# Kernel tuning notes

Hardware: AMD Instinct MI355X
Metric: run time of the kernel (lower is better)

Reference implementation:

```python
import jax, jax.numpy as jnp
import numpy as np

B = 65536
OBS_DIM = 85          # input_shape
FEAT = 8              # dim_entity_feature
NL = 5                # dim_landmarks
NT = 10               # dim_total
INF = 64              # in_features == out_features
HID = 64              # rnn_hidden_dim
NACT = 5              # n_actions
ALPHA = 0.01


def _leaky(x):
    return jnp.where(x > 0, x, ALPHA * x)


def setup_inputs() -> dict:
    key = jax.random.key(0)
    ks = jax.random.split(key, 26)
    s = 0.1
    d = {
        'obs': jax.random.normal(ks[0], (B, OBS_DIM), jnp.float32),
        'hidden_state': jax.random.normal(ks[1], (B, HID), jnp.float32),
        # entity input projections (input_layer_0/1/2), stored [in, out]
        'w_in0': jax.random.normal(ks[2], (FEAT, INF), jnp.float32) * s,
        'b_in0': jax.random.normal(ks[3], (INF,), jnp.float32) * s,
        'w_in1': jax.random.normal(ks[4], (FEAT, INF), jnp.float32) * s,
        'b_in1': jax.random.normal(ks[5], (INF,), jnp.float32) * s,
        'w_in2': jax.random.normal(ks[6], (FEAT, INF), jnp.float32) * s,
        'b_in2': jax.random.normal(ks[7], (INF,), jnp.float32) * s,
        # GAT params
        'W': jax.random.normal(ks[8], (INF, INF), jnp.float32) * s,
        'a': jax.random.normal(ks[9], (2 * INF, 1), jnp.float32) * s,
        # output MLP on attention rows (dim_soft = 2*dim_nearby = 10)
        'w_o1': jax.random.normal(ks[10], (2 * NL, 32), jnp.float32) * s,
        'b_o1': jax.random.normal(ks[11], (32,), jnp.float32) * s,
        'w_o2': jax.random.normal(ks[12], (32, 16), jnp.float32) * s,
        'b_o2': jax.random.normal(ks[13], (16,), jnp.float32) * s,
        'w_o3': jax.random.normal(ks[14], (16, 1), jnp.float32) * s,
        'b_o3': jax.random.normal(ks[15], (1,), jnp.float32) * s,
        # fc1 takes obs (85) concat atom_plug (5) -> 90
        'w_fc1': jax.random.normal(ks[16], (OBS_DIM + NL, HID), jnp.float32) * s,
        'b_fc1': jax.random.normal(ks[17], (HID,), jnp.float32) * s,
        # GRUCell, torch layout: [3H, in]
        'w_ih': jax.random.normal(ks[18], (3 * HID, HID), jnp.float32) * s,
        'w_hh': jax.random.normal(ks[19], (3 * HID, HID), jnp.float32) * s,
        'b_ih': jax.random.normal(ks[20], (3 * HID,), jnp.float32) * s,
        'b_hh': jax.random.normal(ks[21], (3 * HID,), jnp.float32) * s,
        'w_fc2': jax.random.normal(ks[22], (HID, NACT), jnp.float32) * s,
        'b_fc2': jax.random.normal(ks[23], (NACT,), jnp.float32) * s,
    }
    return d


def reference(obs, hidden_state, w_in0, b_in0, w_in1, b_in1, w_in2, b_in2,
              W, a, w_o1, b_o1, w_o2, b_o2, w_o3, b_o3,
              w_fc1, b_fc1, w_ih, w_hh, b_ih, b_hh, w_fc2, b_fc2):
    # data_preprocess: drop last dim_nearby cols, rotate first 4 to back, reshape to entities
    o = obs[:, :OBS_DIM - NL]                               # [B, 80]
    obs_in = jnp.concatenate([o[:, 4:], o[:, :4]], axis=-1).reshape(-1, NT, FEAT)  # [B,10,8]

    h0 = _leaky(obs_in @ w_in0 + b_in0)                     # [B,10,64]
    h1 = _leaky(obs_in @ w_in1 + b_in1)
    h2 = _leaky(obs_in @ w_in2 + b_in2)
    h_mix = jnp.concatenate([h0[:, :NL], h1[:, NL:NT - 1], h2[:, NT - 1:NT]], axis=1)  # [B,10,64]

    Wh = h_mix @ W                                          # [B,10,64]
    Wh1 = Wh @ a[:INF]                                      # [B,10,1]
    Wh2 = Wh @ a[INF:]                                      # [B,10,1]
    e = _leaky(Wh1 + jnp.swapaxes(Wh2, 1, 2))               # [B,10,10]

    att0 = jax.nn.softmax(e[:, :NL, NL:], axis=-1)          # [B,5,5]
    att1 = jnp.swapaxes(jax.nn.softmax(e[:, NL:, :NL], axis=-1), 1, 2)  # [B,5,5]
    attention = jnp.concatenate([att0, att1], axis=-1)      # [B,5,10]

    hp = _leaky(attention @ w_o1 + b_o1)
    hp = _leaky(hp @ w_o2 + b_o2)
    hp = _leaky(hp @ w_o3 + b_o3)[..., 0]                   # [B,5]
    obs_out = jax.nn.softmax(hp, axis=-1)                   # [B,5]

    obs_comb = jnp.concatenate([obs, obs_out], axis=-1)     # [B,90]
    x = jax.nn.relu(obs_comb @ w_fc1 + b_fc1)               # [B,64]

    h_in = hidden_state.reshape(-1, HID)
    gi = x @ w_ih.T + b_ih                                  # [B,192]
    gh = h_in @ w_hh.T + b_hh
    r = jax.nn.sigmoid(gi[:, :HID] + gh[:, :HID])
    z = jax.nn.sigmoid(gi[:, HID:2 * HID] + gh[:, HID:2 * HID])
    n = jnp.tanh(gi[:, 2 * HID:] + r * gh[:, 2 * HID:])
    h = (1.0 - z) * n + z * h_in                            # [B,64]

    q = h @ w_fc2 + b_fc2                                   # [B,5]
    return (q, h)
```

## Files before the change

kernel.cpp:

```cpp
#include <hip/hip_runtime.h>
#include <math.h>

namespace {

typedef __bf16 bf16x8 __attribute__((ext_vector_type(8)));
typedef __bf16 bf16x4 __attribute__((ext_vector_type(4)));
typedef float  f32x4  __attribute__((ext_vector_type(4)));
typedef float  f32x2  __attribute__((ext_vector_type(2)));

typedef __attribute__((address_space(1))) const char GChar;
typedef __attribute__((address_space(3))) char LChar;

constexpr int B_      = 65536;
constexpr int OBS_DIM_= 85;
constexpr int NL_     = 5;
constexpr int NT_     = 10;
constexpr int HID_    = 64;
constexpr int NACT_   = 5;
constexpr float ALPHA_= 0.01f;

__device__ __forceinline__ float leaky(float x)    { return fmaf(fminf(x, 0.0f), ALPHA_ - 1.0f, x); }
__device__ __forceinline__ float sigmoidf(float x) { return 1.0f / (1.0f + __expf(-x)); }
__device__ __forceinline__ float tanh_fast(float x){ return 1.0f - 2.0f / (__expf(2.0f * x) + 1.0f); }

__global__ void prep_kernel(const float* __restrict__ W, const float* __restrict__ a,
                            const float* __restrict__ w_ih, const float* __restrict__ w_hh,
                            const float* __restrict__ w_fc1, void* __restrict__ ws) {
  float* Wa   = (float*)ws;
  __bf16* ih  = (__bf16*)((char*)ws + 512);
  __bf16* hh  = ih + 192 * 64;
  __bf16* f1t = hh + 192 * 64;
  const int tid = blockIdx.x * 256 + threadIdx.x;
  if (blockIdx.x == 0 && threadIdx.x < 64) {
    const int i = threadIdx.x;
    float s1 = 0.0f, s2 = 0.0f;
    #pragma unroll
    for (int j = 0; j < 64; ++j) {
      float w = W[i * 64 + j];
      s1 += w * a[j];
      s2 += w * a[64 + j];
    }
    Wa[i] = s1;
    Wa[64 + i] = s2;
  }
  const int stride = gridDim.x * 256;
  for (int i = tid; i < 192 * 64; i += stride) {
    int pr = i >> 6, k = i & 63;
    int g  = pr >> 6;
    int q  = pr & 63;
    int orig = (g << 6) + ((q & 15) << 2) + (q >> 4);
    ih[i] = (__bf16)w_ih[orig * 64 + k];
    hh[i] = (__bf16)w_hh[orig * 64 + k];
  }
  for (int i = tid; i < 64 * 96; i += stride) {
    int n = i / 96, k = i - 96 * n;
    f1t[i] = (__bf16)(k < 90 ? w_fc1[k * 64 + n] : 0.0f);
  }
}

constexpr int SXH_ = 72;

__global__ __launch_bounds__(256, 2) void fused_kernel(
    const float* __restrict__ obs, const float* __restrict__ hidden,
    const float* __restrict__ w_in0, const float* __restrict__ b_in0,
    const float* __restrict__ w_in1, const float* __restrict__ b_in1,
    const float* __restrict__ w_in2, const float* __restrict__ b_in2,
    const float* __restrict__ w_o1, const float* __restrict__ b_o1,
    const float* __restrict__ w_o2, const float* __restrict__ b_o2,
    const float* __restrict__ w_o3, const float* __restrict__ b_o3,
    const float* __restrict__ b_fc1,
    const float* __restrict__ b_ih, const float* __restrict__ b_hh,
    const float* __restrict__ w_fc2, const float* __restrict__ b_fc2,
    const void* __restrict__ wsv,
    float* __restrict__ q_out, float* __restrict__ h_out) {

  __shared__ __align__(16) char smem[39168];
  float* s_obs = (float*)smem;
  float  (*s_att)[5][10] = (float (*)[5][10])(smem + 21760);
  __bf16 (*s_h1)[5][32]  = (__bf16 (*)[5][32])(smem + 24960);
  float  (*s_h2)[5][16]  = (float (*)[5][16])(smem + 30080);
  __bf16* A_x            = (__bf16*)(smem + 21760);
  float (*s_wh1)[12]     = (float (*)[12])(smem + 35200);
  float (*s_wh2)[12]     = (float (*)[12])(smem + 35968);
  float (*s_colm)[6]     = (float (*)[6])(smem + 36736);
  float (*s_cols)[6]     = (float (*)[6])(smem + 37120);
  float (*s_hp)[6]       = (float (*)[6])(smem + 37504);
  float* s_o5            = (float*)(smem + 37888);

  const int tid  = threadIdx.x;
  const int wv   = tid >> 6;
  const int lane = tid & 63;
  const int l16  = lane & 15;
  const int grp  = tid >> 4;
  const long gr0 = (long)blockIdx.x * 64;

  const float* Wa = (const float*)wsv;
  const __bf16* Wih = (const __bf16*)((const char*)wsv + 512);
  const __bf16* Whh = Wih + 192 * 64;
  const __bf16* Wf1 = Whh + 192 * 64;

  {
    const char* gbase = (const char*)(obs + gr0 * OBS_DIM_) + wv * 5440;
    char* lbase = smem + wv * 5440;
    #pragma unroll
    for (int j = 0; j < 5; ++j)
      __builtin_amdgcn_global_load_lds((const GChar*)(gbase + j * 1024 + lane * 16),
                                       (LChar*)(lbase + j * 1024 + lane * 16), 16, 0, 0);
    if (lane < 20)
      __builtin_amdgcn_global_load_lds((const GChar*)(gbase + 5120 + lane * 16),
                                       (LChar*)(lbase + 5120 + lane * 16), 16, 0, 0);
  }

  const int u0 = l16 * 4;
  const f32x4 wa1 = *(const f32x4*)&Wa[u0];
  const f32x4 wa2 = *(const f32x4*)&Wa[64 + u0];

  asm volatile("s_waitcnt vmcnt(0)" ::: "memory");
  __syncthreads();

  #pragma unroll 1
  for (int pass = 0; pass < 4; ++pass) {
    const int row = pass * 16 + grp;
    const float* orow = s_obs + row * OBS_DIM_;

    f32x4 wA[8];
    f32x4 bA;
    #pragma unroll
    for (int t = 0; t < NT_; ++t) {
      if (t == 0) {
        #pragma unroll
        for (int f = 0; f < 8; ++f) wA[f] = *(const f32x4*)&w_in0[f * 64 + u0];
        bA = *(const f32x4*)&b_in0[u0];
      }
      if (t == 5) {
        #pragma unroll
        for (int f = 0; f < 8; ++f) wA[f] = *(const f32x4*)&w_in1[f * 64 + u0];
        bA = *(const f32x4*)&b_in1[u0];
      }
      if (t == 9) {
        #pragma unroll
        for (int f = 0; f < 8; ++f) wA[f] = *(const f32x4*)&w_in2[f * 64 + u0];
        bA = *(const f32x4*)&b_in2[u0];
      }
      const int ia = t * 8 + 4;
      int ib = t * 8 + 8;
      if (ib >= 80) ib = 0;
      float oa[4], ob[4];
      #pragma unroll
      for (int e = 0; e < 4; ++e) { oa[e] = orow[ia + e]; ob[e] = orow[ib + e]; }
      f32x4 z = bA;
      #pragma unroll
      for (int f = 0; f < 4; ++f) {
        z[0] += oa[f] * wA[f][0]; z[1] += oa[f] * wA[f][1];
        z[2] += oa[f] * wA[f][2]; z[3] += oa[f] * wA[f][3];
      }
      #pragma unroll
      for (int f = 4; f < 8; ++f) {
        z[0] += ob[f - 4] * wA[f][0]; z[1] += ob[f - 4] * wA[f][1];
        z[2] += ob[f - 4] * wA[f][2]; z[3] += ob[f - 4] * wA[f][3];
      }
      float h0 = leaky(z[0]), h1 = leaky(z[1]), h2 = leaky(z[2]), h3 = leaky(z[3]);
      float p1t = h0 * wa1[0] + h1 * wa1[1] + h2 * wa1[2] + h3 * wa1[3];
      float p2t = h0 * wa2[0] + h1 * wa2[1] + h2 * wa2[2] + h3 * wa2[3];
      p1t += __shfl_xor(p1t, 1, 64);  p2t += __shfl_xor(p2t, 1, 64);
      p1t += __shfl_xor(p1t, 2, 64);  p2t += __shfl_xor(p2t, 2, 64);
      p1t += __shfl_xor(p1t, 4, 64);  p2t += __shfl_xor(p2t, 4, 64);
      p1t += __shfl_xor(p1t, 8, 64);  p2t += __shfl_xor(p2t, 8, 64);
      if (l16 == 0) { s_wh1[grp][t] = p1t; s_wh2[grp][t] = p2t; }
    }

    if (l16 >= 5 && l16 < 10) {
      const int jj = l16 - 5;
      float w1v = s_wh1[grp][NL_ + jj];
      float ev[NL_], m = -1e30f;
      #pragma unroll
      for (int k = 0; k < NL_; ++k) { ev[k] = leaky(w1v + s_wh2[grp][k]); m = fmaxf(m, ev[k]); }
      float s = 0.0f;
      #pragma unroll
      for (int k = 0; k < NL_; ++k) s += __expf(ev[k] - m);
      s_colm[grp][jj] = m;
      s_cols[grp][jj] = s;
    }

    if (l16 < NL_) {
      const int r = l16;
      const float wh1_r = s_wh1[grp][r];
      const float wh2_r = s_wh2[grp][r];
      float ev[NL_], m = -1e30f;
      #pragma unroll
      for (int j = 0; j < NL_; ++j) { ev[j] = leaky(wh1_r + s_wh2[grp][NL_ + j]); m = fmaxf(m, ev[j]); }
      float a0[NL_], s = 0.0f;
      #pragma unroll
      for (int j = 0; j < NL_; ++j) { a0[j] = __expf(ev[j] - m); s += a0[j]; }
      float inv = 1.0f / s;
      #pragma unroll
      for (int j = 0; j < NL_; ++j) s_att[grp][r][j] = a0[j] * inv;
      #pragma unroll
      for (int jj = 0; jj < NL_; ++jj) {
        float e = leaky(s_wh1[grp][NL_ + jj] + wh2_r);
        s_att[grp][r][NL_ + jj] = __expf(e - s_colm[grp][jj]) / s_cols[grp][jj];
      }
    }

    {
      f32x2 w1c[NT_];
      #pragma unroll
      for (int k = 0; k < NT_; ++k) w1c[k] = *(const f32x2*)&w_o1[k * 32 + l16 * 2];
      const f32x2 b1 = *(const f32x2*)&b_o1[l16 * 2];
      #pragma unroll
      for (int r5 = 0; r5 < NL_; ++r5) {
        float za = b1[0], zb = b1[1];
        #pragma unroll
        for (int k2 = 0; k2 < 5; ++k2) {
          f32x2 at = *(const f32x2*)&s_att[grp][r5][k2 * 2];
          za += at[0] * w1c[2 * k2][0] + at[1] * w1c[2 * k2 + 1][0];
          zb += at[0] * w1c[2 * k2][1] + at[1] * w1c[2 * k2 + 1][1];
        }
        s_h1[grp][r5][l16 * 2]     = (__bf16)leaky(za);
        s_h1[grp][r5][l16 * 2 + 1] = (__bf16)leaky(zb);
      }
    }

    {
      float w2c[32];
      #pragma unroll
      for (int k = 0; k < 32; ++k) w2c[k] = w_o2[k * 16 + l16];
      const float b2 = b_o2[l16];
      #pragma unroll
      for (int r5 = 0; r5 < NL_; ++r5) {
        float z = b2;
        #pragma unroll
        for (int k4 = 0; k4 < 8; ++k4) {
          bf16x4 hv = *(const bf16x4*)&s_h1[grp][r5][k4 * 4];
          z += (float)hv[0] * w2c[4 * k4] + (float)hv[1] * w2c[4 * k4 + 1]
             + (float)hv[2] * w2c[4 * k4 + 2] + (float)hv[3] * w2c[4 * k4 + 3];
        }
        s_h2[grp][r5][l16] = leaky(z);
      }
    }

    if (l16 < NL_) {
      float z3 = b_o3[0];
      #pragma unroll
      for (int k4 = 0; k4 < 4; ++k4) {
        f32x4 hv = *(const f32x4*)&s_h2[grp][l16][k4 * 4];
        z3 += hv[0] * w_o3[4 * k4] + hv[1] * w_o3[4 * k4 + 1]
            + hv[2] * w_o3[4 * k4 + 2] + hv[3] * w_o3[4 * k4 + 3];
      }
      float hp_own = leaky(z3);
      s_hp[grp][l16] = hp_own;
      float m5 = -1e30f;
      #pragma unroll
      for (int j = 0; j < NL_; ++j) m5 = fmaxf(m5, s_hp[grp][j]);
      float ssum = 0.0f;
      #pragma unroll
      for (int j = 0; j < NL_; ++j) ssum += __expf(s_hp[grp][j] - m5);
      s_o5[row * NL_ + l16] = __expf(hp_own - m5) / ssum;
    }
  }

  __syncthreads();

  const int l    = l16;
  const int quad = lane >> 4;
  const int r0   = wv * 16;

  bf16x8 ah[2];
  {
    const float* hrow_g = hidden + (gr0 + r0 + l) * HID_;
    f32x4 vha0 = *(const f32x4*)&hrow_g[quad * 8];
    f32x4 vha1 = *(const f32x4*)&hrow_g[quad * 8 + 4];
    f32x4 vhb0 = *(const f32x4*)&hrow_g[32 + quad * 8];
    f32x4 vhb1 = *(const f32x4*)&hrow_g[32 + quad * 8 + 4];
    bf16x8 t;
    t[0] = (__bf16)vha0[0]; t[1] = (__bf16)vha0[1]; t[2] = (__bf16)vha0[2]; t[3] = (__bf16)vha0[3];
    t[4] = (__bf16)vha1[0]; t[5] = (__bf16)vha1[1]; t[6] = (__bf16)vha1[2]; t[7] = (__bf16)vha1[3];
    ah[0] = t;
    t[0] = (__bf16)vhb0[0]; t[1] = (__bf16)vhb0[1]; t[2] = (__bf16)vhb0[2]; t[3] = (__bf16)vhb0[3];
    t[4] = (__bf16)vhb1[0]; t[5] = (__bf16)vhb1[1]; t[6] = (__bf16)vhb1[2]; t[7] = (__bf16)vhb1[3];
    ah[1] = t;
  }

  const f32x4 zero4 = {0.0f, 0.0f, 0.0f, 0.0f};
  const float* myrow = s_obs + (r0 + l) * OBS_DIM_;
  const float* myo5  = s_o5 + (r0 + l) * NL_;

  f32x4 cx[4];
  #pragma unroll
  for (int nt = 0; nt < 4; ++nt) cx[nt] = zero4;
  #pragma unroll
  for (int ks = 0; ks < 3; ++ks) {
    bf16x8 af;
    if (ks < 2) {
      const int cb = ks * 32 + quad * 8;
      #pragma unroll
      for (int j = 0; j < 8; ++j) af[j] = (__bf16)myrow[cb + j];
    } else {
      if (quad < 2) {
        const int cb = 64 + quad * 8;
        #pragma unroll
        for (int j = 0; j < 8; ++j) af[j] = (__bf16)myrow[cb + j];
      } else if (quad == 2) {
        #pragma unroll
        for (int j = 0; j < 5; ++j) af[j] = (__bf16)myrow[80 + j];
        #pragma unroll
        for (int j = 5; j < 8; ++j) af[j] = (__bf16)myo5[j - 5];
      } else {
        af[0] = (__bf16)myo5[3];
        af[1] = (__bf16)myo5[4];
        #pragma unroll
        for (int j = 2; j < 8; ++j) af[j] = (__bf16)0.0f;
      }
    }
    #pragma unroll
    for (int nt = 0; nt < 4; ++nt) {
      bf16x8 bf = *(const bf16x8*)&Wf1[(nt * 16 + l) * 96 + ks * 32 + quad * 8];
      cx[nt] = __builtin_amdgcn_mfma_f32_16x16x32_bf16(af, bf, cx[nt], 0, 0, 0);
    }
  }
  #pragma unroll
  for (int nt = 0; nt < 4; ++nt) {
    float bias = b_fc1[nt * 16 + l];
    #pragma unroll
    for (int rg = 0; rg < 4; ++rg) {
      float xv = fmaxf(cx[nt][rg] + bias, 0.0f);
      A_x[(r0 + quad * 4 + rg) * SXH_ + nt * 16 + l] = (__bf16)xv;
    }
  }

  bf16x8 ax[2];
  #pragma unroll
  for (int ks = 0; ks < 2; ++ks)
    ax[ks] = *(const bf16x8*)&A_x[(r0 + l) * SXH_ + ks * 32 + quad * 8];

  f32x4 cr[4], ch[4];
  #pragma unroll
  for (int nt = 0; nt < 4; ++nt) { cr[nt] = zero4; ch[nt] = zero4; }
  #pragma unroll
  for (int nt = 0; nt < 4; ++nt) {
    #pragma unroll
    for (int ks = 0; ks < 2; ++ks) {
      bf16x8 bi = *(const bf16x8*)&Wih[(nt * 16 + l) * 64 + ks * 32 + quad * 8];
      cr[nt] = __builtin_amdgcn_mfma_f32_16x16x32_bf16(ax[ks], bi, cr[nt], 0, 0, 0);
      bf16x8 bh = *(const bf16x8*)&Whh[(nt * 16 + l) * 64 + ks * 32 + quad * 8];
      cr[nt] = __builtin_amdgcn_mfma_f32_16x16x32_bf16(ah[ks], bh, cr[nt], 0, 0, 0);
    }
    #pragma unroll
    for (int ks = 0; ks < 2; ++ks) {
      bf16x8 bh = *(const bf16x8*)&Whh[(128 + nt * 16 + l) * 64 + ks * 32 + quad * 8];
      ch[nt] = __builtin_amdgcn_mfma_f32_16x16x32_bf16(ah[ks], bh, ch[nt], 0, 0, 0);
    }
  }
  f32x4 rn[4];
  {
    f32x4 a0 = *(const f32x4*)&b_ih[4 * l];
    f32x4 a1 = *(const f32x4*)&b_hh[4 * l];
    f32x4 br4 = a0 + a1;
    f32x4 bhn4 = *(const f32x4*)&b_hh[128 + 4 * l];
    #pragma unroll
    for (int nt = 0; nt < 4; ++nt)
      #pragma unroll
      for (int rg = 0; rg < 4; ++rg) {
        float rr = sigmoidf(cr[nt][rg] + br4[nt]);
        rn[nt][rg] = rr * (ch[nt][rg] + bhn4[nt]);
      }
  }

  f32x4 cn[4];
  #pragma unroll
  for (int nt = 0; nt < 4; ++nt) cn[nt] = zero4;
  #pragma unroll
  for (int nt = 0; nt < 4; ++nt)
    #pragma unroll
    for (int ks = 0; ks < 2; ++ks) {
      bf16x8 bi = *(const bf16x8*)&Wih[(128 + nt * 16 + l) * 64 + ks * 32 + quad * 8];
      cn[nt] = __builtin_amdgcn_mfma_f32_16x16x32_bf16(ax[ks], bi, cn[nt], 0, 0, 0);
    }
  f32x4 nn[4];
  {
    f32x4 bin4 = *(const f32x4*)&b_ih[128 + 4 * l];
    #pragma unroll
    for (int nt = 0; nt < 4; ++nt)
      #pragma unroll
      for (int rg = 0; rg < 4; ++rg)
        nn[nt][rg] = tanh_fast(cn[nt][rg] + bin4[nt] + rn[nt][rg]);
  }

  f32x4 cz[4];
  #pragma unroll
  for (int nt = 0; nt < 4; ++nt) cz[nt] = zero4;
  #pragma unroll
  for (int nt = 0; nt < 4; ++nt)
    #pragma unroll
    for (int ks = 0; ks < 2; ++ks) {
      bf16x8 bi = *(const bf16x8*)&Wih[(64 + nt * 16 + l) * 64 + ks * 32 + quad * 8];
      cz[nt] = __builtin_amdgcn_mfma_f32_16x16x32_bf16(ax[ks], bi, cz[nt], 0, 0, 0);
      bf16x8 bh = *(const bf16x8*)&Whh[(64 + nt * 16 + l) * 64 + ks * 32 + quad * 8];
      cz[nt] = __builtin_amdgcn_mfma_f32_16x16x32_bf16(ah[ks], bh, cz[nt], 0, 0, 0);
    }

  const long grow = gr0 + r0 + quad * 4;
  f32x4 bz4;
  {
    f32x4 a0 = *(const f32x4*)&b_ih[64 + 4 * l];
    f32x4 a1 = *(const f32x4*)&b_hh[64 + 4 * l];
    bz4 = a0 + a1;
  }
  f32x4 w20[5];
  #pragma unroll
  for (int j = 0; j < 5; ++j) w20[j] = *(const f32x4*)&w_fc2[20 * l + 4 * j];

  #pragma unroll
  for (int rg = 0; rg < 4; ++rg) {
    f32x4 hold = *(const f32x4*)&hidden[(grow + rg) * HID_ + 4 * l];
    f32x4 hnew;
    float qp5[NACT_] = {0.0f, 0.0f, 0.0f, 0.0f, 0.0f};
    #pragma unroll
    for (int t = 0; t < 4; ++t) {
      float zz = sigmoidf(cz[t][rg] + bz4[t]);
      float hn = (1.0f - zz) * nn[t][rg] + zz * hold[t];
      hnew[t] = hn;
      #pragma unroll
      for (int c = 0; c < NACT_; ++c)
        qp5[c] += hn * w20[(5 * t + c) >> 2][(5 * t + c) & 3];
    }
    *(f32x4*)&h_out[(grow + rg) * HID_ + 4 * l] = hnew;
    #pragma unroll
    for (int m = 1; m < 16; m <<= 1) {
      #pragma unroll
      for (int c = 0; c < NACT_; ++c) qp5[c] += __shfl_xor(qp5[c], m, 64);
    }
    if (l < NACT_) {
      float qv = qp5[0];
      if (l == 1) qv = qp5[1];
      if (l == 2) qv = qp5[2];
      if (l == 3) qv = qp5[3];
      if (l == 4) qv = qp5[4];
      q_out[(grow + rg) * NACT_ + l] = qv + b_fc2[l];
    }
  }
}

}

extern "C" void kernel_launch(void* const* d_in, const int* in_sizes, int n_in,
                              void* d_out, int out_size, void* d_ws, size_t ws_size,
                              hipStream_t stream) {
  const float* obs    = (const float*)d_in[0];
  const float* hidden = (const float*)d_in[1];
  const float* w_in0  = (const float*)d_in[2];
  const float* b_in0  = (const float*)d_in[3];
  const float* w_in1  = (const float*)d_in[4];
  const float* b_in1  = (const float*)d_in[5];
  const float* w_in2  = (const float*)d_in[6];
  const float* b_in2  = (const float*)d_in[7];
  const float* W      = (const float*)d_in[8];
  const float* a      = (const float*)d_in[9];
  const float* w_o1   = (const float*)d_in[10];
  const float* b_o1   = (const float*)d_in[11];
  const float* w_o2   = (const float*)d_in[12];
  const float* b_o2   = (const float*)d_in[13];
  const float* w_o3   = (const float*)d_in[14];
  const float* b_o3   = (const float*)d_in[15];
  const float* w_fc1  = (const float*)d_in[16];
  const float* b_fc1  = (const float*)d_in[17];
  const float* w_ih   = (const float*)d_in[18];
  const float* w_hh   = (const float*)d_in[19];
  const float* b_ih   = (const float*)d_in[20];
  const float* b_hh   = (const float*)d_in[21];
  const float* w_fc2  = (const float*)d_in[22];
  const float* b_fc2  = (const float*)d_in[23];

  float* q_out = (float*)d_out;
  float* h_out = q_out + (long)B_ * NACT_;

  prep_kernel<<<48, 256, 0, stream>>>(W, a, w_ih, w_hh, w_fc1, d_ws);
  fused_kernel<<<B_ / 64, 256, 0, stream>>>(
      obs, hidden,
      w_in0, b_in0, w_in1, b_in1, w_in2, b_in2,
      w_o1, b_o1, w_o2, b_o2, w_o3, b_o3,
      b_fc1, b_ih, b_hh, w_fc2, b_fc2,
      d_ws, q_out, h_out);
}
```

Baseline: 198.3 us.

## Stage obs as padded bf16 in LDS and use DPP reductions

Obs rows are now loaded through registers, converted to bf16 and stored in LDS with a padded 88-element stride, replacing the async global-to-LDS fp32 copy. The padding lets the MFMA A-fragments load as single bf16x8 vectors, and the fc1 weight layout is reordered to match. Sixteen-lane butterfly reductions now use DPP row operations instead of shuffles. LDS use drops, which may allow more blocks per CU. The cost is that the entity projection now reads bf16-rounded obs, adding precision loss, and the direct global-to-LDS path is lost.

```diff
diff --git a/kernel.cpp b/kernel.cpp
--- a/kernel.cpp
+++ b/kernel.cpp
@@ -7,9 +7,6 @@
 typedef __bf16 bf16x4 __attribute__((ext_vector_type(4)));
 typedef float  f32x4  __attribute__((ext_vector_type(4)));
 typedef float  f32x2  __attribute__((ext_vector_type(2)));
-
-typedef __attribute__((address_space(1))) const char GChar;
-typedef __attribute__((address_space(3))) char LChar;
 
 constexpr int B_      = 65536;
 constexpr int OBS_DIM_= 85;
@@ -22,6 +19,19 @@
 __device__ __forceinline__ float leaky(float x)    { return fmaf(fminf(x, 0.0f), ALPHA_ - 1.0f, x); }
 __device__ __forceinline__ float sigmoidf(float x) { return 1.0f / (1.0f + __expf(-x)); }
 __device__ __forceinline__ float tanh_fast(float x){ return 1.0f - 2.0f / (__expf(2.0f * x) + 1.0f); }
+
+template <int CTRL>
+__device__ __forceinline__ float dppadd(float x) {
+  int y = __builtin_amdgcn_update_dpp(0, __float_as_int(x), CTRL, 0xF, 0xF, true);
+  return x + __int_as_float(y);
+}
+__device__ __forceinline__ float red16(float x) {
+  x = dppadd<0xB1>(x);
+  x = dppadd<0x4E>(x);
+  x = dppadd<0x141>(x);
+  x = dppadd<0x140>(x);
+  return x;
+}
 
 __global__ void prep_kernel(const float* __restrict__ W, const float* __restrict__ a,
                             const float* __restrict__ w_ih, const float* __restrict__ w_hh,
@@ -54,7 +64,10 @@
   }
   for (int i = tid; i < 64 * 96; i += stride) {
     int n = i / 96, k = i - 96 * n;
-    f1t[i] = (__bf16)(k < 90 ? w_fc1[k * 64 + n] : 0.0f);
+    float v = 0.0f;
+    if (k < 85)                 v = w_fc1[k * 64 + n];
+    else if (k >= 88 && k < 93) v = w_fc1[(85 + k - 88) * 64 + n];
+    f1t[i] = (__bf16)v;
   }
 }
 
@@ -74,18 +87,18 @@
     const void* __restrict__ wsv,
     float* __restrict__ q_out, float* __restrict__ h_out) {
 
-  __shared__ __align__(16) char smem[39168];
-  float* s_obs = (float*)smem;
-  float  (*s_att)[5][10] = (float (*)[5][10])(smem + 21760);
-  __bf16 (*s_h1)[5][32]  = (__bf16 (*)[5][32])(smem + 24960);
-  float  (*s_h2)[5][16]  = (float (*)[5][16])(smem + 30080);
-  __bf16* A_x            = (__bf16*)(smem + 21760);
-  float (*s_wh1)[12]     = (float (*)[12])(smem + 35200);
-  float (*s_wh2)[12]     = (float (*)[12])(smem + 35968);
-  float (*s_colm)[6]     = (float (*)[6])(smem + 36736);
-  float (*s_cols)[6]     = (float (*)[6])(smem + 37120);
-  float (*s_hp)[6]       = (float (*)[6])(smem + 37504);
-  float* s_o5            = (float*)(smem + 37888);
+  __shared__ __align__(16) char smem[28416];
+  __bf16* s_obs          = (__bf16*)smem;
+  float  (*s_att)[5][10] = (float (*)[5][10])(smem + 11264);
+  __bf16 (*s_h1)[5][32]  = (__bf16 (*)[5][32])(smem + 14464);
+  float  (*s_h2)[5][16]  = (float (*)[5][16])(smem + 19584);
+  __bf16* A_x            = (__bf16*)(smem + 11264);
+  float (*s_wh1)[12]     = (float (*)[12])(smem + 24704);
+  float (*s_wh2)[12]     = (float (*)[12])(smem + 25472);
+  float (*s_colm)[6]     = (float (*)[6])(smem + 26240);
+  float (*s_cols)[6]     = (float (*)[6])(smem + 26624);
+  float (*s_hp)[6]       = (float (*)[6])(smem + 27008);
+  __bf16* s_o5           = (__bf16*)(smem + 27392);
 
   const int tid  = threadIdx.x;
   const int wv   = tid >> 6;
@@ -100,28 +113,38 @@
   const __bf16* Wf1 = Whh + 192 * 64;
 
   {
-    const char* gbase = (const char*)(obs + gr0 * OBS_DIM_) + wv * 5440;
-    char* lbase = smem + wv * 5440;
-    #pragma unroll
-    for (int j = 0; j < 5; ++j)
-      __builtin_amdgcn_global_load_lds((const GChar*)(gbase + j * 1024 + lane * 16),
-                                       (LChar*)(lbase + j * 1024 + lane * 16), 16, 0, 0);
-    if (lane < 20)
-      __builtin_amdgcn_global_load_lds((const GChar*)(gbase + 5120 + lane * 16),
-                                       (LChar*)(lbase + 5120 + lane * 16), 16, 0, 0);
+    const float* src = obs + gr0 * OBS_DIM_;
+    const int base = wv * 340;
+    #pragma unroll
+    for (int k = 0; k < 6; ++k) {
+      if (k < 5 || lane < 20) {
+        int c = base + k * 64 + lane;
+        f32x4 v = *(const f32x4*)&src[c * 4];
+        #pragma unroll
+        for (int e = 0; e < 4; ++e) {
+          int fe = c * 4 + e;
+          int r = fe / 85, col = fe - 85 * r;
+          s_obs[r * 88 + col] = (__bf16)v[e];
+        }
+      }
+    }
+    if (lane < 48) {
+      int r = wv * 16 + lane / 3, j = lane % 3;
+      s_obs[r * 88 + 85 + j] = (__bf16)0.0f;
+      s_o5[r * 8 + 5 + j]    = (__bf16)0.0f;
+    }
   }
 
   const int u0 = l16 * 4;
   const f32x4 wa1 = *(const f32x4*)&Wa[u0];
   const f32x4 wa2 = *(const f32x4*)&Wa[64 + u0];
 
-  asm volatile("s_waitcnt vmcnt(0)" ::: "memory");
   __syncthreads();
 
   #pragma unroll 1
   for (int pass = 0; pass < 4; ++pass) {
     const int row = pass * 16 + grp;
-    const float* orow = s_obs + row * OBS_DIM_;
+    const __bf16* orow = s_obs + row * 88;
 
     f32x4 wA[8];
     f32x4 bA;
@@ -145,9 +168,11 @@
       const int ia = t * 8 + 4;
       int ib = t * 8 + 8;
       if (ib >= 80) ib = 0;
+      bf16x4 va = *(const bf16x4*)&orow[ia];
+      bf16x4 vb = *(const bf16x4*)&orow[ib];
       float oa[4], ob[4];
       #pragma unroll
-      for (int e = 0; e < 4; ++e) { oa[e] = orow[ia + e]; ob[e] = orow[ib + e]; }
+      for (int e = 0; e < 4; ++e) { oa[e] = (float)va[e]; ob[e] = (float)vb[e]; }
       f32x4 z = bA;
       #pragma unroll
       for (int f = 0; f < 4; ++f) {
@@ -162,10 +187,8 @@
       float h0 = leaky(z[0]), h1 = leaky(z[1]), h2 = leaky(z[2]), h3 = leaky(z[3]);
       float p1t = h0 * wa1[0] + h1 * wa1[1] + h2 * wa1[2] + h3 * wa1[3];
       float p2t = h0 * wa2[0] + h1 * wa2[1] + h2 * wa2[2] + h3 * wa2[3];
-      p1t += __shfl_xor(p1t, 1, 64);  p2t += __shfl_xor(p2t, 1, 64);
-      p1t += __shfl_xor(p1t, 2, 64);  p2t += __shfl_xor(p2t, 2, 64);
-      p1t += __shfl_xor(p1t, 4, 64);  p2t += __shfl_xor(p2t, 4, 64);
-      p1t += __shfl_xor(p1t, 8, 64);  p2t += __shfl_xor(p2t, 8, 64);
+      p1t = red16(p1t);
+      p2t = red16(p2t);
       if (l16 == 0) { s_wh1[grp][t] = p1t; s_wh2[grp][t] = p2t; }
     }
 
@@ -255,7 +278,7 @@
       float ssum = 0.0f;
       #pragma unroll
       for (int j = 0; j < NL_; ++j) ssum += __expf(s_hp[grp][j] - m5);
-      s_o5[row * NL_ + l16] = __expf(hp_own - m5) / ssum;
+      s_o5[row * 8 + l16] = (__bf16)(__expf(hp_own - m5) / ssum);
     }
   }
 
@@ -282,8 +305,6 @@
   }
 
   const f32x4 zero4 = {0.0f, 0.0f, 0.0f, 0.0f};
-  const float* myrow = s_obs + (r0 + l) * OBS_DIM_;
-  const float* myo5  = s_o5 + (r0 + l) * NL_;
 
   f32x4 cx[4];
   #pragma unroll
@@ -291,27 +312,9 @@
   #pragma unroll
   for (int ks = 0; ks < 3; ++ks) {
     bf16x8 af;
-    if (ks < 2) {
-      const int cb = ks * 32 + quad * 8;
-      #pragma unroll
-      for (int j = 0; j < 8; ++j) af[j] = (__bf16)myrow[cb + j];
-    } else {
-      if (quad < 2) {
-        const int cb = 64 + quad * 8;
-        #pragma unroll
-        for (int j = 0; j < 8; ++j) af[j] = (__bf16)myrow[cb + j];
-      } else if (quad == 2) {
-        #pragma unroll
-        for (int j = 0; j < 5; ++j) af[j] = (__bf16)myrow[80 + j];
-        #pragma unroll
-        for (int j = 5; j < 8; ++j) af[j] = (__bf16)myo5[j - 5];
-      } else {
-        af[0] = (__bf16)myo5[3];
-        af[1] = (__bf16)myo5[4];
-        #pragma unroll
-        for (int j = 2; j < 8; ++j) af[j] = (__bf16)0.0f;
-      }
-    }
+    if (ks < 2)         af = *(const bf16x8*)&s_obs[(r0 + l) * 88 + ks * 32 + quad * 8];
+    else if (quad < 3)  af = *(const bf16x8*)&s_obs[(r0 + l) * 88 + 64 + quad * 8];
+    else                af = *(const bf16x8*)&s_o5[(r0 + l) * 8];
     #pragma unroll
     for (int nt = 0; nt < 4; ++nt) {
       bf16x8 bf = *(const bf16x8*)&Wf1[(nt * 16 + l) * 96 + ks * 32 + quad * 8];
@@ -426,10 +429,7 @@
     }
     *(f32x4*)&h_out[(grow + rg) * HID_ + 4 * l] = hnew;
     #pragma unroll
-    for (int m = 1; m < 16; m <<= 1) {
-      #pragma unroll
-      for (int c = 0; c < NACT_; ++c) qp5[c] += __shfl_xor(qp5[c], m, 64);
-    }
+    for (int c = 0; c < NACT_; ++c) qp5[c] = red16(qp5[c]);
     if (l < NACT_) {
       float qv = qp5[0];
       if (l == 1) qv = qp5[1];
```

Measured after the change: 190.3 us, median of 3. 4.0% less time.
